# Performance work log

Measured on AMD Instinct MI355X. Metric: run time of the kernel, lower is better.

Reference implementation:

```python
import jax, jax.numpy as jnp
import numpy as np

HEAD_SIZE = 64

def setup_inputs() -> dict:
    key = jax.random.key(0)
    kx, kk, kq, kv = jax.random.split(key, 4)
    B, T, C, H = 8, 2048, 1024, HEAD_SIZE
    scale = 1.0 / np.sqrt(C)
    x = jax.random.normal(kx, (B, T, C), dtype=jnp.float32)
    # nn.Linear(n_emb, head_size, bias=False) weights, shape (head_size, n_emb)
    Wk = jax.random.normal(kk, (H, C), dtype=jnp.float32) * scale
    Wq = jax.random.normal(kq, (H, C), dtype=jnp.float32) * scale
    Wv = jax.random.normal(kv, (H, C), dtype=jnp.float32) * scale
    return {"x": x, "Wk": Wk, "Wq": Wq, "Wv": Wv}

def reference(x, Wk, Wq, Wv):
    # x: (B,T,C); W*: (H,C). Single causal self-attention head.
    H = Wk.shape[0]
    k = jnp.einsum('btc,hc->bth', x, Wk)
    q = jnp.einsum('btc,hc->bth', x, Wq)
    v = jnp.einsum('btc,hc->bth', x, Wv)
    scores = jnp.einsum('bth,bsh->bts', q, k) / jnp.sqrt(jnp.float32(H))
    T = x.shape[1]
    causal = jnp.tril(jnp.ones((T, T), dtype=bool))  # (T,T)
    scores = jnp.where(causal, scores, -jnp.inf)
    attn = jax.nn.softmax(scores, axis=-1)
    out = jnp.einsum('bts,bsh->bth', attn, v)  # (B,T,H)
    return out
```

## Files before the change

kernel.cpp:

```cpp
#include <hip/hip_runtime.h>
#include <hip/hip_bf16.h>

typedef __bf16 bf16_t;
typedef __bf16 bf16x8 __attribute__((ext_vector_type(8)));
typedef float  f32x4  __attribute__((ext_vector_type(4)));

#define B_ 8
#define T_ 2048
#define C_ 1024
#define H_ 64

#define MFMA16(a, b, c) __builtin_amdgcn_mfma_f32_16x16x32_bf16((a), (b), (c), 0, 0, 0)
#define GLL16(g, l) __builtin_amdgcn_global_load_lds( \
    (const __attribute__((address_space(1))) unsigned int*)(g), \
    (__attribute__((address_space(3))) unsigned int*)(l), 16, 0, 0)
#define SBAR() asm volatile("s_barrier" ::: "memory")

__global__ __launch_bounds__(256) void wconv_kernel(
    const float* __restrict__ Wk, const float* __restrict__ Wq,
    const float* __restrict__ Wv,
    bf16_t* __restrict__ Wh, bf16_t* __restrict__ Wl,
    f32x4* __restrict__ zero_dst)
{
    int i = blockIdx.x * 256 + threadIdx.x;
    zero_dst[i] = (f32x4){0.f, 0.f, 0.f, 0.f};
    if (blockIdx.x < 768) {
        int r = i >> 10;
        int c = i & 1023;
        float v;
        if (r < 64)       v = Wq[r * 1024 + c];
        else if (r < 128) v = Wk[(r - 64) * 1024 + c];
        else              v = Wv[(r - 128) * 1024 + c];
        bf16_t h = (bf16_t)v;
        Wh[i] = h;
        Wl[i] = (bf16_t)(v - (float)h);
    }
}

__global__ __launch_bounds__(512, 4) void proj_kernel(
    const float*  __restrict__ x,
    const bf16_t* __restrict__ Wh, const bf16_t* __restrict__ Wl,
    bf16_t* __restrict__ qh, bf16_t* __restrict__ ql,
    bf16_t* __restrict__ kh, bf16_t* __restrict__ kl,
    bf16_t* __restrict__ vh)
{
    __shared__ bf16_t Wlds[2][24][512];

    const int tid   = threadIdx.x;
    const int wid   = tid >> 6;
    const int lane  = tid & 63;
    const int quad  = lane >> 4;
    const int l16   = lane & 15;
    const int mhalf = wid >> 2;
    const int nq    = wid & 3;
    const int g     = blockIdx.x * 32 + mhalf * 16 + l16;
    const float* xrow = x + (size_t)g * C_;

    auto stage = [&](int k0, int bufi) {
        #pragma unroll
        for (int i = 0; i < 3; ++i) {
            int grp = wid * 3 + i;
            int mat = (grp >= 12);
            int nt  = grp - mat * 12;
            const bf16_t* src = (mat ? Wl : Wh) + (nt * 16 + l16) * 1024 + k0 + quad * 8;
            GLL16(src, &Wlds[bufi][grp][0]);
        }
    };
    auto loadx = [&](int it, f32x4* d) {
        d[0] = *(const f32x4*)(xrow + it * 32 + quad * 8);
        d[1] = *(const f32x4*)(xrow + it * 32 + quad * 8 + 4);
    };

    stage(0, 0);
    f32x4 x0[2], x1[2];
    loadx(0, x0);
    loadx(1, x1);

    f32x4 acc[3];
    #pragma unroll
    for (int i = 0; i < 3; ++i) acc[i] = (f32x4){0.f, 0.f, 0.f, 0.f};

    int buf = 0;
    for (int it = 0; it < 32; ++it) {
        float xv[8];
        *(f32x4*)(xv)     = x0[0];
        *(f32x4*)(xv + 4) = x0[1];
        x0[0] = x1[0]; x0[1] = x1[1];

        if (it + 1 < 32) {
            stage((it + 1) * 32, buf ^ 1);
            if (it + 2 < 32) {
                loadx(it + 2, x1);
                asm volatile("s_waitcnt vmcnt(5)" ::: "memory");
            } else {
                asm volatile("s_waitcnt vmcnt(3)" ::: "memory");
            }
        } else {
            asm volatile("s_waitcnt vmcnt(0)" ::: "memory");
        }
        SBAR();

        bf16x8 ah, al;
        #pragma unroll
        for (int jj = 0; jj < 8; ++jj) {
            bf16_t h = (bf16_t)xv[jj];
            ah[jj] = h;
            al[jj] = (bf16_t)(xv[jj] - (float)h);
        }

        #pragma unroll
        for (int nt = 0; nt < 3; ++nt) {
            int gi = nq * 3 + nt;
            bf16x8 bh = *(const bf16x8*)(&Wlds[buf][gi][lane * 8]);
            bf16x8 bl = *(const bf16x8*)(&Wlds[buf][gi + 12][lane * 8]);
            acc[nt] = MFMA16(ah, bh, acc[nt]);
            acc[nt] = MFMA16(ah, bl, acc[nt]);
            acc[nt] = MFMA16(al, bh, acc[nt]);
        }

        SBAR();
        buf ^= 1;
    }

    const int rowbase = blockIdx.x * 32 + mhalf * 16 + quad * 4;
    for (int nt = 0; nt < 3; ++nt) {
        int n = (nq * 3 + nt) * 16 + l16;
        for (int rr = 0; rr < 4; ++rr) {
            int grow = rowbase + rr;
            int bb = grow >> 11, t = grow & 2047;
            float v  = acc[nt][rr];
            bf16_t h = (bf16_t)v;
            if (n < 64) {
                int off = (bb * T_ + t) * H_ + n;
                qh[off] = h; ql[off] = (bf16_t)(v - (float)h);
            } else if (n < 128) {
                int off = (bb * T_ + t) * H_ + (n - 64);
                kh[off] = h; kl[off] = (bf16_t)(v - (float)h);
            } else {
                vh[(bb * H_ + (n - 128)) * T_ + t] = h;
            }
        }
    }
}

__global__ __launch_bounds__(512, 4) void attn_kernel(
    const bf16_t* __restrict__ qh, const bf16_t* __restrict__ ql,
    const bf16_t* __restrict__ kh, const bf16_t* __restrict__ kl,
    const bf16_t* __restrict__ vh,
    float* __restrict__ Oacc, float* __restrict__ lacc)
{
    __shared__ bf16_t KV[2][3][4096];
    __shared__ bf16_t Plds[8][16 * 72];

    const int tid  = threadIdx.x;
    const int wid  = tid >> 6;
    const int lane = tid & 63;
    const int quad = lane >> 4;
    const int l16  = lane & 15;

    const int b  = blockIdx.x & 7;
    const int gp = (blockIdx.x >> 3) & 7;
    const int s  = blockIdx.x >> 6;
    const int gA = gp, gB = 15 - gp;
    const int nA = 2 * gA + 2;

    const int t_nt   = wid >> 1;
    const int t_kk   = wid & 1;
    const int t_l16  = tid & 15;
    const int t_quad = (tid >> 4) & 3;
    const int koff   = (t_nt * 16 + t_l16) * H_ + t_kk * 32 + t_quad * 8;
    const int voff   = (t_nt * 16 + t_l16) * T_ + t_kk * 32 + t_quad * 8;

    auto stage = [&](int j, int bufi) {
        const size_t kbase = (size_t)(b * T_ + 64 * j) * H_;
        GLL16(kh + kbase + koff, &KV[bufi][0][wid * 512]);
        GLL16(kl + kbase + koff, &KV[bufi][1][wid * 512]);
        GLL16(vh + (size_t)b * H_ * T_ + 64 * j + voff, &KV[bufi][2][wid * 512]);
    };

    f32x4  O[4];
    float  rowsum[4];
    bf16x8 aqh[2], aql[2];
    int    gcur = -1;

    auto flushO = [&]() {
        #pragma unroll
        for (int rr = 0; rr < 4; ++rr) {
            int trow = b * T_ + 128 * gcur + 16 * wid + quad * 4 + rr;
            #pragma unroll
            for (int ht = 0; ht < 4; ++ht)
                atomicAdd(Oacc + (size_t)trow * H_ + ht * 16 + l16, O[ht][rr]);
            float s_ = rowsum[rr];
            s_ += __shfl_xor(s_, 1, 64);
            s_ += __shfl_xor(s_, 2, 64);
            s_ += __shfl_xor(s_, 4, 64);
            s_ += __shfl_xor(s_, 8, 64);
            if (l16 == 0) atomicAdd(lacc + trow, s_);
        }
    };

    {
        int u0 = s;
        int j0 = (u0 < nA) ? u0 : (u0 - nA);
        stage(j0, 0);
    }

    int buf = 0;
    for (int u = s; u < 34; u += 8) {
        const int g = (u < nA) ? gA : gB;
        const int j = (u < nA) ? u : (u - nA);

        const int un = u + 8;
        if (un < 34) {
            int jn = (un < nA) ? un : (un - nA);
            stage(jn, buf ^ 1);
            asm volatile("s_waitcnt vmcnt(3)" ::: "memory");
        } else {
            asm volatile("s_waitcnt vmcnt(0)" ::: "memory");
        }
        SBAR();

        if (g != gcur) {
            if (gcur >= 0) flushO();
            gcur = g;
            const size_t qoff = (size_t)(b * T_ + 128 * g + 16 * wid + l16) * H_;
            #pragma unroll
            for (int kk = 0; kk < 2; ++kk) {
                aqh[kk] = *(const bf16x8*)(qh + qoff + kk * 32 + quad * 8);
                aql[kk] = *(const bf16x8*)(ql + qoff + kk * 32 + quad * 8);
            }
            #pragma unroll
            for (int i = 0; i < 4; ++i) { O[i] = (f32x4){0.f,0.f,0.f,0.f}; rowsum[i] = 0.f; }
        }

        const bf16_t* Kh = KV[buf][0];
        const bf16_t* Kl = KV[buf][1];
        f32x4 S[4];
        #pragma unroll
        for (int i = 0; i < 4; ++i) S[i] = (f32x4){0.f,0.f,0.f,0.f};
        #pragma unroll
        for (int nt = 0; nt < 4; ++nt) {
            #pragma unroll
            for (int kk = 0; kk < 2; ++kk) {
                bf16x8 bh = *(const bf16x8*)(Kh + (nt * 2 + kk) * 512 + lane * 8);
                bf16x8 bl = *(const bf16x8*)(Kl + (nt * 2 + kk) * 512 + lane * 8);
                S[nt] = MFMA16(aqh[kk], bh, S[nt]);
                S[nt] = MFMA16(aqh[kk], bl, S[nt]);
                S[nt] = MFMA16(aql[kk], bh, S[nt]);
            }
        }

        bf16_t* Pw = Plds[wid];
        const int rloc = 128 * g + 16 * wid + quad * 4;
        #pragma unroll
        for (int nt = 0; nt < 4; ++nt) {
            int colt = 64 * j + nt * 16 + l16;
            #pragma unroll
            for (int rr = 0; rr < 4; ++rr) {
                float pv = (colt <= rloc + rr)
                         ? __expf(fmaf(S[nt][rr], 0.125f, -20.0f)) : 0.f;
                rowsum[rr] += pv;
                Pw[(quad * 4 + rr) * 72 + nt * 16 + l16] = (bf16_t)pv;
            }
        }

        bf16x8 ap0 = *(const bf16x8*)(Pw + l16 * 72 + quad * 8);
        bf16x8 ap1 = *(const bf16x8*)(Pw + l16 * 72 + 32 + quad * 8);

        const bf16_t* Vt = KV[buf][2];
        #pragma unroll
        for (int ht = 0; ht < 4; ++ht) {
            bf16x8 bv0 = *(const bf16x8*)(Vt + (ht * 2 + 0) * 512 + lane * 8);
            bf16x8 bv1 = *(const bf16x8*)(Vt + (ht * 2 + 1) * 512 + lane * 8);
            O[ht] = MFMA16(ap0, bv0, O[ht]);
            O[ht] = MFMA16(ap1, bv1, O[ht]);
        }

        SBAR();
        buf ^= 1;
    }
    if (gcur >= 0) flushO();
}

__global__ __launch_bounds__(256) void div_kernel(
    const float* __restrict__ Oacc, const float* __restrict__ lacc,
    float* __restrict__ out)
{
    int i = blockIdx.x * 256 + threadIdx.x;
    f32x4 o   = ((const f32x4*)Oacc)[i];
    float inv = 1.0f / lacc[i >> 4];
    ((f32x4*)out)[i] = o * inv;
}

extern "C" void kernel_launch(void* const* d_in, const int* in_sizes, int n_in,
                              void* d_out, int out_size, void* d_ws, size_t ws_size,
                              hipStream_t stream)
{
    const float* x  = (const float*)d_in[0];
    const float* Wk = (const float*)d_in[1];
    const float* Wq = (const float*)d_in[2];
    const float* Wv = (const float*)d_in[3];
    float* out = (float*)d_out;

    char* ws = (char*)d_ws;
    const size_t WSZ = 192 * 1024 * sizeof(bf16_t);
    const size_t QSZ = (size_t)B_ * T_ * H_ * sizeof(bf16_t);
    bf16_t* Wh   = (bf16_t*)(ws);
    bf16_t* Wl   = (bf16_t*)(ws + WSZ);
    bf16_t* qh   = (bf16_t*)(ws + 2 * WSZ);
    bf16_t* ql   = (bf16_t*)(ws + 2 * WSZ + 1 * QSZ);
    bf16_t* kh   = (bf16_t*)(ws + 2 * WSZ + 2 * QSZ);
    bf16_t* kl   = (bf16_t*)(ws + 2 * WSZ + 3 * QSZ);
    bf16_t* vh   = (bf16_t*)(ws + 2 * WSZ + 4 * QSZ);
    float*  Oacc = (float*)(ws + 2 * WSZ + 5 * QSZ);
    float*  lacc = (float*)(ws + 2 * WSZ + 5 * QSZ + (size_t)B_ * T_ * H_ * 4);

    hipLaunchKernelGGL(wconv_kernel, dim3(1040), dim3(256), 0, stream,
                       Wk, Wq, Wv, Wh, Wl, (f32x4*)Oacc);
    hipLaunchKernelGGL(proj_kernel, dim3(512), dim3(512), 0, stream,
                       x, Wh, Wl, qh, ql, kh, kl, vh);
    hipLaunchKernelGGL(attn_kernel, dim3(512), dim3(512), 0, stream,
                       qh, ql, kh, kl, vh, Oacc, lacc);
    hipLaunchKernelGGL(div_kernel, dim3(1024), dim3(256), 0, stream, Oacc, lacc, out);
}
```

Before: 197.6 us.

## Fuse all four kernels into one persistent kernel with grid barriers

Merges weight conversion, projection, attention and the final normalization into a single launch, separated by software grid barriers built on an atomic counter. Weights are now read as fp32 and split into bf16 hi/lo inside each block, using a 3-slot LDS ring instead of a separate pre-conversion kernel. The Oacc/lacc zeroing also moves into the projection phase. This removes launch overhead and the intermediate weight buffers, but relies on all 512 blocks being co-resident and adds redundant per-block weight conversion plus an extra memset launch.

```diff
diff --git a/kernel.cpp b/kernel.cpp
--- a/kernel.cpp
+++ b/kernel.cpp
@@ -16,141 +16,30 @@
     (__attribute__((address_space(3))) unsigned int*)(l), 16, 0, 0)
 #define SBAR() asm volatile("s_barrier" ::: "memory")
 
-__global__ __launch_bounds__(256) void wconv_kernel(
+__device__ __forceinline__ void grid_barrier(unsigned* ctr, unsigned target)
+{
+    __syncthreads();
+    __threadfence();
+    if (threadIdx.x == 0) {
+        __hip_atomic_fetch_add(ctr, 1u, __ATOMIC_RELEASE, __HIP_MEMORY_SCOPE_AGENT);
+        while (__hip_atomic_load(ctr, __ATOMIC_ACQUIRE, __HIP_MEMORY_SCOPE_AGENT) < target)
+            __builtin_amdgcn_s_sleep(2);
+    }
+    __syncthreads();
+    __threadfence();
+}
+
+__global__ __launch_bounds__(512, 4) void fused_kernel(
+    const float* __restrict__ x,
     const float* __restrict__ Wk, const float* __restrict__ Wq,
     const float* __restrict__ Wv,
-    bf16_t* __restrict__ Wh, bf16_t* __restrict__ Wl,
-    f32x4* __restrict__ zero_dst)
-{
-    int i = blockIdx.x * 256 + threadIdx.x;
-    zero_dst[i] = (f32x4){0.f, 0.f, 0.f, 0.f};
-    if (blockIdx.x < 768) {
-        int r = i >> 10;
-        int c = i & 1023;
-        float v;
-        if (r < 64)       v = Wq[r * 1024 + c];
-        else if (r < 128) v = Wk[(r - 64) * 1024 + c];
-        else              v = Wv[(r - 128) * 1024 + c];
-        bf16_t h = (bf16_t)v;
-        Wh[i] = h;
-        Wl[i] = (bf16_t)(v - (float)h);
-    }
-}
-
-__global__ __launch_bounds__(512, 4) void proj_kernel(
-    const float*  __restrict__ x,
-    const bf16_t* __restrict__ Wh, const bf16_t* __restrict__ Wl,
     bf16_t* __restrict__ qh, bf16_t* __restrict__ ql,
     bf16_t* __restrict__ kh, bf16_t* __restrict__ kl,
-    bf16_t* __restrict__ vh)
+    bf16_t* __restrict__ vh,
+    float* __restrict__ Oacc, float* __restrict__ lacc,
+    float* __restrict__ out, unsigned* __restrict__ ctr)
 {
-    __shared__ bf16_t Wlds[2][24][512];
-
-    const int tid   = threadIdx.x;
-    const int wid   = tid >> 6;
-    const int lane  = tid & 63;
-    const int quad  = lane >> 4;
-    const int l16   = lane & 15;
-    const int mhalf = wid >> 2;
-    const int nq    = wid & 3;
-    const int g     = blockIdx.x * 32 + mhalf * 16 + l16;
-    const float* xrow = x + (size_t)g * C_;
-
-    auto stage = [&](int k0, int bufi) {
-        #pragma unroll
-        for (int i = 0; i < 3; ++i) {
-            int grp = wid * 3 + i;
-            int mat = (grp >= 12);
-            int nt  = grp - mat * 12;
-            const bf16_t* src = (mat ? Wl : Wh) + (nt * 16 + l16) * 1024 + k0 + quad * 8;
-            GLL16(src, &Wlds[bufi][grp][0]);
-        }
-    };
-    auto loadx = [&](int it, f32x4* d) {
-        d[0] = *(const f32x4*)(xrow + it * 32 + quad * 8);
-        d[1] = *(const f32x4*)(xrow + it * 32 + quad * 8 + 4);
-    };
-
-    stage(0, 0);
-    f32x4 x0[2], x1[2];
-    loadx(0, x0);
-    loadx(1, x1);
-
-    f32x4 acc[3];
-    #pragma unroll
-    for (int i = 0; i < 3; ++i) acc[i] = (f32x4){0.f, 0.f, 0.f, 0.f};
-
-    int buf = 0;
-    for (int it = 0; it < 32; ++it) {
-        float xv[8];
-        *(f32x4*)(xv)     = x0[0];
-        *(f32x4*)(xv + 4) = x0[1];
-        x0[0] = x1[0]; x0[1] = x1[1];
-
-        if (it + 1 < 32) {
-            stage((it + 1) * 32, buf ^ 1);
-            if (it + 2 < 32) {
-                loadx(it + 2, x1);
-                asm volatile("s_waitcnt vmcnt(5)" ::: "memory");
-            } else {
-                asm volatile("s_waitcnt vmcnt(3)" ::: "memory");
-            }
-        } else {
-            asm volatile("s_waitcnt vmcnt(0)" ::: "memory");
-        }
-        SBAR();
-
-        bf16x8 ah, al;
-        #pragma unroll
-        for (int jj = 0; jj < 8; ++jj) {
-            bf16_t h = (bf16_t)xv[jj];
-            ah[jj] = h;
-            al[jj] = (bf16_t)(xv[jj] - (float)h);
-        }
-
-        #pragma unroll
-        for (int nt = 0; nt < 3; ++nt) {
-            int gi = nq * 3 + nt;
-            bf16x8 bh = *(const bf16x8*)(&Wlds[buf][gi][lane * 8]);
-            bf16x8 bl = *(const bf16x8*)(&Wlds[buf][gi + 12][lane * 8]);
-            acc[nt] = MFMA16(ah, bh, acc[nt]);
-            acc[nt] = MFMA16(ah, bl, acc[nt]);
-            acc[nt] = MFMA16(al, bh, acc[nt]);
-        }
-
-        SBAR();
-        buf ^= 1;
-    }
-
-    const int rowbase = blockIdx.x * 32 + mhalf * 16 + quad * 4;
-    for (int nt = 0; nt < 3; ++nt) {
-        int n = (nq * 3 + nt) * 16 + l16;
-        for (int rr = 0; rr < 4; ++rr) {
-            int grow = rowbase + rr;
-            int bb = grow >> 11, t = grow & 2047;
-            float v  = acc[nt][rr];
-            bf16_t h = (bf16_t)v;
-            if (n < 64) {
-                int off = (bb * T_ + t) * H_ + n;
-                qh[off] = h; ql[off] = (bf16_t)(v - (float)h);
-            } else if (n < 128) {
-                int off = (bb * T_ + t) * H_ + (n - 64);
-                kh[off] = h; kl[off] = (bf16_t)(v - (float)h);
-            } else {
-                vh[(bb * H_ + (n - 128)) * T_ + t] = h;
-            }
-        }
-    }
-}
-
-__global__ __launch_bounds__(512, 4) void attn_kernel(
-    const bf16_t* __restrict__ qh, const bf16_t* __restrict__ ql,
-    const bf16_t* __restrict__ kh, const bf16_t* __restrict__ kl,
-    const bf16_t* __restrict__ vh,
-    float* __restrict__ Oacc, float* __restrict__ lacc)
-{
-    __shared__ bf16_t KV[2][3][4096];
-    __shared__ bf16_t Plds[8][16 * 72];
+    __shared__ __attribute__((aligned(16))) char smem[73728];
 
     const int tid  = threadIdx.x;
     const int wid  = tid >> 6;
@@ -158,138 +47,274 @@
     const int quad = lane >> 4;
     const int l16  = lane & 15;
 
-    const int b  = blockIdx.x & 7;
-    const int gp = (blockIdx.x >> 3) & 7;
-    const int s  = blockIdx.x >> 6;
-    const int gA = gp, gB = 15 - gp;
-    const int nA = 2 * gA + 2;
-
-    const int t_nt   = wid >> 1;
-    const int t_kk   = wid & 1;
-    const int t_l16  = tid & 15;
-    const int t_quad = (tid >> 4) & 3;
-    const int koff   = (t_nt * 16 + t_l16) * H_ + t_kk * 32 + t_quad * 8;
-    const int voff   = (t_nt * 16 + t_l16) * T_ + t_kk * 32 + t_quad * 8;
-
-    auto stage = [&](int j, int bufi) {
-        const size_t kbase = (size_t)(b * T_ + 64 * j) * H_;
-        GLL16(kh + kbase + koff, &KV[bufi][0][wid * 512]);
-        GLL16(kl + kbase + koff, &KV[bufi][1][wid * 512]);
-        GLL16(vh + (size_t)b * H_ * T_ + 64 * j + voff, &KV[bufi][2][wid * 512]);
-    };
-
-    f32x4  O[4];
-    float  rowsum[4];
-    bf16x8 aqh[2], aql[2];
-    int    gcur = -1;
-
-    auto flushO = [&]() {
+    {
+        bf16_t* Wlds0 = (bf16_t*)smem;
+        const int mhalf = wid >> 2;
+        const int nq    = wid & 3;
+        const int g     = blockIdx.x * 32 + mhalf * 16 + l16;
+        const float* xrow = x + (size_t)g * C_;
+
+        const int nck = (tid < 256) ? 2 : 1;
+        const float* ck_src[2] = {nullptr, nullptr};
+        int ck_hi[2] = {0, 0}, ck_lo[2] = {0, 0};
+        for (int i = 0; i < nck; ++i) {
+            int ci = tid + 512 * i;
+            int nt = ci >> 6, ln = ci & 63;
+            int row = nt * 16 + (ln & 15);
+            const float* base = (row < 64)  ? Wq + row * 1024
+                              : (row < 128) ? Wk + (row - 64) * 1024
+                                            : Wv + (row - 128) * 1024;
+            ck_src[i] = base + (ln >> 4) * 8;
+            ck_hi[i]  = nt * 512 + ln * 8;
+            ck_lo[i]  = (nt + 12) * 512 + ln * 8;
+        }
+
+        f32x4 wr[4];
+        auto loadW = [&](int it) {
+            for (int i = 0; i < nck; ++i) {
+                wr[i * 2]     = *(const f32x4*)(ck_src[i] + it * 32);
+                wr[i * 2 + 1] = *(const f32x4*)(ck_src[i] + it * 32 + 4);
+            }
+        };
+        auto convertWrite = [&](int slot) {
+            bf16_t* L = Wlds0 + slot * (24 * 512);
+            for (int i = 0; i < nck; ++i) {
+                float wf[8];
+                *(f32x4*)(wf)     = wr[i * 2];
+                *(f32x4*)(wf + 4) = wr[i * 2 + 1];
+                bf16x8 hv, lv;
+                #pragma unroll
+                for (int j = 0; j < 8; ++j) {
+                    bf16_t h = (bf16_t)wf[j];
+                    hv[j] = h;
+                    lv[j] = (bf16_t)(wf[j] - (float)h);
+                }
+                *(bf16x8*)(L + ck_hi[i]) = hv;
+                *(bf16x8*)(L + ck_lo[i]) = lv;
+            }
+        };
+        auto loadx = [&](int it, f32x4* d) {
+            d[0] = *(const f32x4*)(xrow + it * 32 + quad * 8);
+            d[1] = *(const f32x4*)(xrow + it * 32 + quad * 8 + 4);
+        };
+
+        f32x4 x0[2], x1[2];
+        loadW(0);
+        loadx(0, x0);
+        loadx(1, x1);
+        asm volatile("s_waitcnt vmcnt(0)" ::: "memory");
+        convertWrite(0);
+        loadW(1);
+        asm volatile("s_waitcnt lgkmcnt(0)" ::: "memory");
+        SBAR();
+
+        f32x4 acc[3];
         #pragma unroll
-        for (int rr = 0; rr < 4; ++rr) {
-            int trow = b * T_ + 128 * gcur + 16 * wid + quad * 4 + rr;
-            #pragma unroll
-            for (int ht = 0; ht < 4; ++ht)
-                atomicAdd(Oacc + (size_t)trow * H_ + ht * 16 + l16, O[ht][rr]);
-            float s_ = rowsum[rr];
-            s_ += __shfl_xor(s_, 1, 64);
-            s_ += __shfl_xor(s_, 2, 64);
-            s_ += __shfl_xor(s_, 4, 64);
-            s_ += __shfl_xor(s_, 8, 64);
-            if (l16 == 0) atomicAdd(lacc + trow, s_);
-        }
-    };
+        for (int i = 0; i < 3; ++i) acc[i] = (f32x4){0.f, 0.f, 0.f, 0.f};
+
+        int slot = 0;
+        for (int it = 0; it < 32; ++it) {
+            const int nslot = (slot == 2) ? 0 : slot + 1;
+            float xv[8];
+            *(f32x4*)(xv)     = x0[0];
+            *(f32x4*)(xv + 4) = x0[1];
+            x0[0] = x1[0]; x0[1] = x1[1];
+
+            asm volatile("s_waitcnt vmcnt(0)" ::: "memory");
+            if (it + 1 < 32) {
+                convertWrite(nslot);
+                if (it + 2 < 32) { loadW(it + 2); loadx(it + 2, x1); }
+            }
+            asm volatile("s_waitcnt lgkmcnt(0)" ::: "memory");
+            SBAR();
+
+            bf16x8 ah, al;
+            #pragma unroll
+            for (int jj = 0; jj < 8; ++jj) {
+                bf16_t h = (bf16_t)xv[jj];
+                ah[jj] = h;
+                al[jj] = (bf16_t)(xv[jj] - (float)h);
+            }
+            const bf16_t* L = Wlds0 + slot * (24 * 512);
+            #pragma unroll
+            for (int nt = 0; nt < 3; ++nt) {
+                int gi = nq * 3 + nt;
+                bf16x8 bh = *(const bf16x8*)(L + gi * 512 + lane * 8);
+                bf16x8 bl = *(const bf16x8*)(L + (gi + 12) * 512 + lane * 8);
+                acc[nt] = MFMA16(ah, bh, acc[nt]);
+                acc[nt] = MFMA16(ah, bl, acc[nt]);
+                acc[nt] = MFMA16(al, bh, acc[nt]);
+            }
+            slot = nslot;
+        }
+
+        const int rowbase = blockIdx.x * 32 + mhalf * 16 + quad * 4;
+        for (int nt = 0; nt < 3; ++nt) {
+            int n = (nq * 3 + nt) * 16 + l16;
+            for (int rr = 0; rr < 4; ++rr) {
+                int grow = rowbase + rr;
+                int bb = grow >> 11, t = grow & 2047;
+                float v  = acc[nt][rr];
+                bf16_t h = (bf16_t)v;
+                if (n < 64) {
+                    int off = (bb * T_ + t) * H_ + n;
+                    qh[off] = h; ql[off] = (bf16_t)(v - (float)h);
+                } else if (n < 128) {
+                    int off = (bb * T_ + t) * H_ + (n - 64);
+                    kh[off] = h; kl[off] = (bf16_t)(v - (float)h);
+                } else {
+                    vh[(bb * H_ + (n - 128)) * T_ + t] = h;
+                }
+            }
+        }
+        {
+            f32x4* Z = (f32x4*)Oacc + (size_t)blockIdx.x * 520;
+            for (int i = tid; i < 520; i += 512)
+                Z[i] = (f32x4){0.f, 0.f, 0.f, 0.f};
+        }
+    }
+
+    grid_barrier(ctr, 512);
 
     {
-        int u0 = s;
-        int j0 = (u0 < nA) ? u0 : (u0 - nA);
-        stage(j0, 0);
+        bf16_t* KVbase = (bf16_t*)smem;
+        bf16_t* Pbase  = (bf16_t*)(smem + 49152);
+        auto kvp = [&](int bufi, int m) -> bf16_t* {
+            return KVbase + (bufi * 3 + m) * 4096;
+        };
+
+        const int b  = blockIdx.x & 7;
+        const int gp = (blockIdx.x >> 3) & 7;
+        const int s  = blockIdx.x >> 6;
+        const int gA = gp, gB = 15 - gp;
+        const int nA = 2 * gA + 2;
+
+        const int t_nt   = wid >> 1;
+        const int t_kk   = wid & 1;
+        const int t_l16  = tid & 15;
+        const int t_quad = (tid >> 4) & 3;
+        const int koff   = (t_nt * 16 + t_l16) * H_ + t_kk * 32 + t_quad * 8;
+        const int voff   = (t_nt * 16 + t_l16) * T_ + t_kk * 32 + t_quad * 8;
+
+        auto stage = [&](int j, int bufi) {
+            const size_t kbase = (size_t)(b * T_ + 64 * j) * H_;
+            GLL16(kh + kbase + koff, kvp(bufi, 0) + wid * 512);
+            GLL16(kl + kbase + koff, kvp(bufi, 1) + wid * 512);
+            GLL16(vh + (size_t)b * H_ * T_ + 64 * j + voff, kvp(bufi, 2) + wid * 512);
+        };
+
+        f32x4  O[4];
+        float  rowsum[4];
+        bf16x8 aqh[2], aql[2];
+        int    gcur = -1;
+
+        auto flushO = [&]() {
+            #pragma unroll
+            for (int rr = 0; rr < 4; ++rr) {
+                int trow = b * T_ + 128 * gcur + 16 * wid + quad * 4 + rr;
+                #pragma unroll
+                for (int ht = 0; ht < 4; ++ht)
+                    atomicAdd(Oacc + (size_t)trow * H_ + ht * 16 + l16, O[ht][rr]);
+                float s_ = rowsum[rr];
+                s_ += __shfl_xor(s_, 1, 64);
+                s_ += __shfl_xor(s_, 2, 64);
+                s_ += __shfl_xor(s_, 4, 64);
+                s_ += __shfl_xor(s_, 8, 64);
+                if (l16 == 0) atomicAdd(lacc + trow, s_);
+            }
+        };
+
+        {
+            int u0 = s;
+            int j0 = (u0 < nA) ? u0 : (u0 - nA);
+            stage(j0, 0);
+        }
+
+        int buf = 0;
+        for (int u = s; u < 34; u += 8) {
+            const int g = (u < nA) ? gA : gB;
+            const int j = (u < nA) ? u : (u - nA);
+
+            const int un = u + 8;
+            if (un < 34) {
+                int jn = (un < nA) ? un : (un - nA);
+                stage(jn, buf ^ 1);
+                asm volatile("s_waitcnt vmcnt(3)" ::: "memory");
+            } else {
+                asm volatile("s_waitcnt vmcnt(0)" ::: "memory");
+            }
+            SBAR();
+
+            if (g != gcur) {
+                if (gcur >= 0) flushO();
+                gcur = g;
+                const size_t qoff = (size_t)(b * T_ + 128 * g + 16 * wid + l16) * H_;
+                #pragma unroll
+                for (int kk = 0; kk < 2; ++kk) {
+                    aqh[kk] = *(const bf16x8*)(qh + qoff + kk * 32 + quad * 8);
+                    aql[kk] = *(const bf16x8*)(ql + qoff + kk * 32 + quad * 8);
+                }
+                #pragma unroll
+                for (int i = 0; i < 4; ++i) { O[i] = (f32x4){0.f,0.f,0.f,0.f}; rowsum[i] = 0.f; }
+            }
+
+            const bf16_t* Kh = kvp(buf, 0);
+            const bf16_t* Kl = kvp(buf, 1);
+            f32x4 S[4];
+            #pragma unroll
+            for (int i = 0; i < 4; ++i) S[i] = (f32x4){0.f,0.f,0.f,0.f};
+            #pragma unroll
+            for (int nt = 0; nt < 4; ++nt) {
+                #pragma unroll
+                for (int kk = 0; kk < 2; ++kk) {
+                    bf16x8 bh = *(const bf16x8*)(Kh + (nt * 2 + kk) * 512 + lane * 8);
+                    bf16x8 bl = *(const bf16x8*)(Kl + (nt * 2 + kk) * 512 + lane * 8);
+                    S[nt] = MFMA16(aqh[kk], bh, S[nt]);
+                    S[nt] = MFMA16(aqh[kk], bl, S[nt]);
+                    S[nt] = MFMA16(aql[kk], bh, S[nt]);
+                }
+            }
+
+            bf16_t* Pw = Pbase + wid * (16 * 72);
+            const int rloc = 128 * g + 16 * wid + quad * 4;
+            #pragma unroll
+            for (int nt = 0; nt < 4; ++nt) {
+                int colt = 64 * j + nt * 16 + l16;
+                #pragma unroll
+                for (int rr = 0; rr < 4; ++rr) {
+                    float pv = (colt <= rloc + rr)
+                             ? __expf(fmaf(S[nt][rr], 0.125f, -20.0f)) : 0.f;
+                    rowsum[rr] += pv;
+                    Pw[(quad * 4 + rr) * 72 + nt * 16 + l16] = (bf16_t)pv;
+                }
+            }
+
+            bf16x8 ap0 = *(const bf16x8*)(Pw + l16 * 72 + quad * 8);
+            bf16x8 ap1 = *(const bf16x8*)(Pw + l16 * 72 + 32 + quad * 8);
+
+            const bf16_t* Vt = kvp(buf, 2);
+            #pragma unroll
+            for (int ht = 0; ht < 4; ++ht) {
+                bf16x8 bv0 = *(const bf16x8*)(Vt + (ht * 2 + 0) * 512 + lane * 8);
+                bf16x8 bv1 = *(const bf16x8*)(Vt + (ht * 2 + 1) * 512 + lane * 8);
+                O[ht] = MFMA16(ap0, bv0, O[ht]);
+                O[ht] = MFMA16(ap1, bv1, O[ht]);
+            }
+
+            SBAR();
+            buf ^= 1;
+        }
+        if (gcur >= 0) flushO();
     }
 
-    int buf = 0;
-    for (int u = s; u < 34; u += 8) {
-        const int g = (u < nA) ? gA : gB;
-        const int j = (u < nA) ? u : (u - nA);
-
-        const int un = u + 8;
-        if (un < 34) {
-            int jn = (un < nA) ? un : (un - nA);
-            stage(jn, buf ^ 1);
-            asm volatile("s_waitcnt vmcnt(3)" ::: "memory");
-        } else {
-            asm volatile("s_waitcnt vmcnt(0)" ::: "memory");
-        }
-        SBAR();
-
-        if (g != gcur) {
-            if (gcur >= 0) flushO();
-            gcur = g;
-            const size_t qoff = (size_t)(b * T_ + 128 * g + 16 * wid + l16) * H_;
-            #pragma unroll
-            for (int kk = 0; kk < 2; ++kk) {
-                aqh[kk] = *(const bf16x8*)(qh + qoff + kk * 32 + quad * 8);
-                aql[kk] = *(const bf16x8*)(ql + qoff + kk * 32 + quad * 8);
-            }
-            #pragma unroll
-            for (int i = 0; i < 4; ++i) { O[i] = (f32x4){0.f,0.f,0.f,0.f}; rowsum[i] = 0.f; }
-        }
-
-        const bf16_t* Kh = KV[buf][0];
-        const bf16_t* Kl = KV[buf][1];
-        f32x4 S[4];
-        #pragma unroll
-        for (int i = 0; i < 4; ++i) S[i] = (f32x4){0.f,0.f,0.f,0.f};
-        #pragma unroll
-        for (int nt = 0; nt < 4; ++nt) {
-            #pragma unroll
-            for (int kk = 0; kk < 2; ++kk) {
-                bf16x8 bh = *(const bf16x8*)(Kh + (nt * 2 + kk) * 512 + lane * 8);
-                bf16x8 bl = *(const bf16x8*)(Kl + (nt * 2 + kk) * 512 + lane * 8);
-                S[nt] = MFMA16(aqh[kk], bh, S[nt]);
-                S[nt] = MFMA16(aqh[kk], bl, S[nt]);
-                S[nt] = MFMA16(aql[kk], bh, S[nt]);
-            }
-        }
-
-        bf16_t* Pw = Plds[wid];
-        const int rloc = 128 * g + 16 * wid + quad * 4;
-        #pragma unroll
-        for (int nt = 0; nt < 4; ++nt) {
-            int colt = 64 * j + nt * 16 + l16;
-            #pragma unroll
-            for (int rr = 0; rr < 4; ++rr) {
-                float pv = (colt <= rloc + rr)
-                         ? __expf(fmaf(S[nt][rr], 0.125f, -20.0f)) : 0.f;
-                rowsum[rr] += pv;
-                Pw[(quad * 4 + rr) * 72 + nt * 16 + l16] = (bf16_t)pv;
-            }
-        }
-
-        bf16x8 ap0 = *(const bf16x8*)(Pw + l16 * 72 + quad * 8);
-        bf16x8 ap1 = *(const bf16x8*)(Pw + l16 * 72 + 32 + quad * 8);
-
-        const bf16_t* Vt = KV[buf][2];
-        #pragma unroll
-        for (int ht = 0; ht < 4; ++ht) {
-            bf16x8 bv0 = *(const bf16x8*)(Vt + (ht * 2 + 0) * 512 + lane * 8);
-            bf16x8 bv1 = *(const bf16x8*)(Vt + (ht * 2 + 1) * 512 + lane * 8);
-            O[ht] = MFMA16(ap0, bv0, O[ht]);
-            O[ht] = MFMA16(ap1, bv1, O[ht]);
-        }
-
-        SBAR();
-        buf ^= 1;
+    grid_barrier(ctr, 1024);
+
+    {
+        int i = blockIdx.x * 512 + tid;
+        f32x4 o   = ((const f32x4*)Oacc)[i];
+        float inv = 1.0f / lacc[i >> 4];
+        ((f32x4*)out)[i] = o * inv;
     }
-    if (gcur >= 0) flushO();
-}
-
-__global__ __launch_bounds__(256) void div_kernel(
-    const float* __restrict__ Oacc, const float* __restrict__ lacc,
-    float* __restrict__ out)
-{
-    int i = blockIdx.x * 256 + threadIdx.x;
-    f32x4 o   = ((const f32x4*)Oacc)[i];
-    float inv = 1.0f / lacc[i >> 4];
-    ((f32x4*)out)[i] = o * inv;
 }
 
 extern "C" void kernel_launch(void* const* d_in, const int* in_sizes, int n_in,
@@ -303,23 +328,18 @@
     float* out = (float*)d_out;
 
     char* ws = (char*)d_ws;
-    const size_t WSZ = 192 * 1024 * sizeof(bf16_t);
     const size_t QSZ = (size_t)B_ * T_ * H_ * sizeof(bf16_t);
-    bf16_t* Wh   = (bf16_t*)(ws);
-    bf16_t* Wl   = (bf16_t*)(ws + WSZ);
-    bf16_t* qh   = (bf16_t*)(ws + 2 * WSZ);
-    bf16_t* ql   = (bf16_t*)(ws + 2 * WSZ + 1 * QSZ);
-    bf16_t* kh   = (bf16_t*)(ws + 2 * WSZ + 2 * QSZ);
-    bf16_t* kl   = (bf16_t*)(ws + 2 * WSZ + 3 * QSZ);
-    bf16_t* vh   = (bf16_t*)(ws + 2 * WSZ + 4 * QSZ);
-    float*  Oacc = (float*)(ws + 2 * WSZ + 5 * QSZ);
-    float*  lacc = (float*)(ws + 2 * WSZ + 5 * QSZ + (size_t)B_ * T_ * H_ * 4);
-
-    hipLaunchKernelGGL(wconv_kernel, dim3(1040), dim3(256), 0, stream,
-                       Wk, Wq, Wv, Wh, Wl, (f32x4*)Oacc);
-    hipLaunchKernelGGL(proj_kernel, dim3(512), dim3(512), 0, stream,
-                       x, Wh, Wl, qh, ql, kh, kl, vh);
-    hipLaunchKernelGGL(attn_kernel, dim3(512), dim3(512), 0, stream,
-                       qh, ql, kh, kl, vh, Oacc, lacc);
-    hipLaunchKernelGGL(div_kernel, dim3(1024), dim3(256), 0, stream, Oacc, lacc, out);
+    bf16_t* qh   = (bf16_t*)(ws);
+    bf16_t* ql   = (bf16_t*)(ws + 1 * QSZ);
+    bf16_t* kh   = (bf16_t*)(ws + 2 * QSZ);
+    bf16_t* kl   = (bf16_t*)(ws + 3 * QSZ);
+    bf16_t* vh   = (bf16_t*)(ws + 4 * QSZ);
+    float*  Oacc = (float*)(ws + 5 * QSZ);
+    float*  lacc = (float*)(ws + 5 * QSZ + (size_t)B_ * T_ * H_ * 4);
+    unsigned* ctr = (unsigned*)(ws + 5 * QSZ
+                                + (size_t)B_ * T_ * H_ * 4 + (size_t)B_ * T_ * 4);
+
+    hipMemsetAsync(ctr, 0, sizeof(unsigned), stream);
+    hipLaunchKernelGGL(fused_kernel, dim3(512), dim3(512), 0, stream,
+                       x, Wk, Wq, Wv, qh, ql, kh, kl, vh, Oacc, lacc, out, ctr);
 }
```

New measurement: 688.2 us. 248% more time.
